# Performance work log

Hardware: AMD Instinct MI355X
Metric: run time of the kernel (lower is better)

The kernel has to match this reference:

```python
import jax, jax.numpy as jnp
import numpy as np

N, E, CIN, A, C, NB, B = 20000, 100000, 64, 32, 256, 4, 128
FD = C * NB  # fusion_dims = channels + c_growth*(n_blocks_out-1) with c_growth==channels
HID = 1024


def setup_inputs() -> dict:
    key = jax.random.key(0)
    ks = jax.random.split(key, 24)
    s = 0.05
    inp = {
        "x": jax.random.normal(ks[0], (N, CIN), jnp.float32),
        "edges": jax.random.randint(ks[1], (2, E), 0, N, jnp.int32),
        "edge_weights": jax.random.uniform(ks[2], (E,), jnp.float32),
        "edge_attrs": jax.random.normal(ks[3], (E, A), jnp.float32),
        "bbox_idx": jax.random.randint(ks[4], (N,), 0, B, jnp.int32),
        "num_boxes": B,
        # head GraphConv params: message MLP on [x_dst, x_src-x_dst, edge_attr]
        "W_msg0": jax.random.normal(ks[5], (2 * CIN + A, C), jnp.float32) * s,
        "b_msg0": jnp.zeros((C,), jnp.float32),
        "W_sup0": jax.random.normal(ks[6], (C + CIN, C), jnp.float32) * s,
        "b_sup0": jnp.zeros((C,), jnp.float32),
        # ResBlock params (n_blocks-1 blocks)
        "W_msg": jax.random.normal(ks[7], (NB - 1, 2 * C + A, C), jnp.float32) * s,
        "b_msg": jnp.zeros((NB - 1, C), jnp.float32),
        "W_sup": jax.random.normal(ks[8], (NB - 1, 2 * C, C), jnp.float32) * s,
        "b_sup": jnp.zeros((NB - 1, C), jnp.float32),
        # fusion MLPs [fusion_dims -> 1024]
        "W_fuse": jax.random.normal(ks[9], (FD, HID), jnp.float32) * s,
        "b_fuse": jnp.zeros((HID,), jnp.float32),
        "W_fuse_sup": jax.random.normal(ks[10], (FD, HID), jnp.float32) * s,
        "b_fuse_sup": jnp.zeros((HID,), jnp.float32),
    }
    return inp


def reference(x, edge_weights, edge_attrs, W_msg0, b_msg0, W_sup0, b_sup0,
              W_msg, b_msg, W_sup, b_sup, W_fuse, b_fuse, W_fuse_sup, b_fuse_sup,
              edges, bbox_idx, num_boxes):
    src, dst = edges[0], edges[1]
    n = x.shape[0]

    def gconv(f_in, Wm, bm):
        # per-edge message on [f_dst, f_src - f_dst, edge_attr], weighted sum-aggregate to dst
        h = jnp.concatenate([f_in[dst], f_in[src] - f_in[dst], edge_attrs], axis=1)
        m = jax.nn.relu(h @ Wm + bm) * edge_weights[:, None]
        return jax.ops.segment_sum(m, dst, num_segments=n)

    def super_node(f, x_node, Ws, bs):
        return jax.nn.relu(jnp.concatenate([f, x_node], axis=1) @ Ws + bs)

    # head GraphConv
    f = gconv(x, W_msg0, b_msg0)
    fs = super_node(f, x, W_sup0, b_sup0)
    feats, feats_super = [f], [fs]
    # ResBlocks: residual on node features, fresh super features
    for i in range(NB - 1):
        f = gconv(feats[-1], W_msg[i], b_msg[i]) + feats[-1]
        fs = super_node(f, feats_super[-1], W_sup[i], b_sup[i])
        feats.append(f)
        feats_super.append(fs)

    # n_blocks_out == n_blocks -> take all blocks
    feats_cat = jnp.concatenate(feats, axis=1)            # [N, FD]
    fusion = jax.nn.relu(feats_cat @ W_fuse + b_fuse)     # [N, 1024]
    out_feat = jnp.concatenate([fusion, feats_cat], axis=1)

    fs_cat = jnp.concatenate(feats_super, axis=1)         # [N, FD]
    sums = jax.ops.segment_sum(fs_cat, bbox_idx, num_segments=num_boxes)
    cnts = jax.ops.segment_sum(jnp.ones((n, 1), fs_cat.dtype), bbox_idx, num_segments=num_boxes)
    fs_mean = sums / jnp.maximum(cnts, 1.0)               # scatter(reduce='mean')
    fusion_sup = jax.nn.relu(fs_mean @ W_fuse_sup + b_fuse_sup)
    out_feat_super = jnp.concatenate([fusion_sup, fs_mean], axis=1)
    return out_feat, out_feat_super
```

## Files before the change

### kernel.cpp

```cpp
#include <hip/hip_runtime.h>

#define N_NODES 20000
#define N_EDGES 100000
#define CIN     64
#define A_DIM   32
#define CCH     256
#define NBOX    128
#define FD      1024
#define HID     1024
#define OUT_STRIDE 2048

typedef __attribute__((ext_vector_type(8))) short          short8;
typedef __attribute__((ext_vector_type(8))) unsigned short ushort8;
typedef __attribute__((ext_vector_type(4))) unsigned short ushort4v;
typedef __attribute__((ext_vector_type(4))) float          floatx4;

__device__ __forceinline__ unsigned short f2bf(float f) {
    unsigned int u = __float_as_uint(f);
    u += 0x7fff + ((u >> 16) & 1);
    return (unsigned short)(u >> 16);
}
__device__ __forceinline__ float bf2f(unsigned short h) {
    return __uint_as_float(((unsigned int)h) << 16);
}

__device__ __forceinline__ void glds16(const unsigned short* g, unsigned short* l) {
    __builtin_amdgcn_global_load_lds(
        (const __attribute__((address_space(1))) unsigned int*)g,
        (__attribute__((address_space(3))) unsigned int*)l,
        16, 0, 0);
}

struct GD {
    const unsigned short* src0b;
    const unsigned short* src1b;
    const unsigned short* Wt;
    const float* bias;
    const int* ridx0;
    float* outf;
    unsigned short* outb;
    int s0, o0, C0, s1, o1, do_relu, sof, oof, sob, oob, rmode, M, K, nbc;
};

__global__ __launch_bounds__(256) void mfma_dense(GD A, GD B, int n0)
{
    __shared__ __align__(16) unsigned short SM[2][4096];

    const int tid = threadIdx.x;
    const bool fa = (int)blockIdx.x < n0;

    const unsigned short* src0b = fa ? A.src0b : B.src0b;
    const unsigned short* src1b = fa ? A.src1b : B.src1b;
    const unsigned short* Wt    = fa ? A.Wt    : B.Wt;
    const float* bias           = fa ? A.bias  : B.bias;
    const int*   ridx0          = fa ? A.ridx0 : B.ridx0;
    float* outf                 = fa ? A.outf  : B.outf;
    unsigned short* outb        = fa ? A.outb  : B.outb;
    const int s0  = fa ? A.s0  : B.s0,  o0  = fa ? A.o0  : B.o0;
    const int C0  = fa ? A.C0  : B.C0;
    const int s1  = fa ? A.s1  : B.s1,  o1  = fa ? A.o1  : B.o1;
    const int do_relu = fa ? A.do_relu : B.do_relu;
    const int sof = fa ? A.sof : B.sof, oof = fa ? A.oof : B.oof;
    const int sob = fa ? A.sob : B.sob, oob = fa ? A.oob : B.oob;
    const int rmode = fa ? A.rmode : B.rmode;
    const int M   = fa ? A.M   : B.M;
    const int K   = fa ? A.K   : B.K;
    const int nbc = fa ? A.nbc : B.nbc;

    const int nwg = fa ? n0 : (int)gridDim.x - n0;
    const int lb  = (int)blockIdx.x - (fa ? 0 : n0);
    const int q8  = nwg >> 3, r8 = nwg & 7;
    const int xcd = lb & 7, boff = lb >> 3;
    const int bid = (xcd < r8 ? xcd * (q8 + 1)
                              : r8 * (q8 + 1) + (xcd - r8) * q8) + boff;

    const int rb   = bid / nbc, cb = bid % nbc;
    const int r0   = rb * 128, c0 = cb * 128;
    const int wave = tid >> 6, lane = tid & 63;
    const int quad = lane >> 4, l16 = lane & 15;
    const int wm   = (wave & 1) * 64, wn = (wave >> 1) * 64;

    int arow[2], grow[2], brow[2], kch[2];
    #pragma unroll
    for (int i = 0; i < 2; ++i) {
        const int g  = i * 256 + tid;
        const int rr = g >> 2;
        kch[i] = (g & 3) << 3;
        int gr2 = r0 + rr;
        if (gr2 >= M) gr2 = M - 1;
        grow[i] = gr2;
        arow[i] = ridx0 ? ridx0[gr2] : gr2;
        brow[i] = c0 + rr;
    }
    unsigned short* AsW = &SM[0][wave * 512];
    unsigned short* BsW = &SM[1][wave * 512];

    floatx4 acc[4][4];
    #pragma unroll
    for (int i = 0; i < 4; ++i)
        #pragma unroll
        for (int j = 0; j < 4; ++j) acc[i][j] = (floatx4){0.f, 0.f, 0.f, 0.f};

    const unsigned short* pB0 = Wt + (long)brow[0] * K + kch[0];
    const unsigned short* pB1 = Wt + (long)brow[1] * K + kch[1];

    auto KSTEP = [&](const unsigned short* pA0, const unsigned short* pA1) {
        glds16(pA0, AsW);
        glds16(pB0, BsW);
        glds16(pA1, AsW + 2048);
        glds16(pB1, BsW + 2048);
        __syncthreads();

        short8 af[4], bfr[4];
        #pragma unroll
        for (int mt = 0; mt < 4; ++mt)
            af[mt] = *(const short8*)(&SM[0][(wm + mt * 16 + l16) * 32 + quad * 8]);
        #pragma unroll
        for (int nt = 0; nt < 4; ++nt)
            bfr[nt] = *(const short8*)(&SM[1][(wn + nt * 16 + l16) * 32 + quad * 8]);
        #pragma unroll
        for (int mt = 0; mt < 4; ++mt)
            #pragma unroll
            for (int nt = 0; nt < 4; ++nt)
                acc[mt][nt] = __builtin_amdgcn_mfma_f32_16x16x32_bf16(
                    af[mt], bfr[nt], acc[mt][nt], 0, 0, 0);
        __syncthreads();
        pB0 += 32; pB1 += 32;
    };

    int k0 = 0;
    const int Ka = (C0 < K) ? C0 : K;
    if (k0 < Ka) {
        const unsigned short* pA0 = src0b + (long)arow[0] * s0 + o0 + kch[0];
        const unsigned short* pA1 = src0b + (long)arow[1] * s0 + o0 + kch[1];
        for (; k0 < Ka; k0 += 32) {
            KSTEP(pA0, pA1);
            pA0 += 32; pA1 += 32;
        }
    }
    if (k0 < K) {
        const unsigned short* pA0 = src1b + (long)grow[0] * s1 + o1 + kch[0];
        const unsigned short* pA1 = src1b + (long)grow[1] * s1 + o1 + kch[1];
        for (; k0 < K; k0 += 32) {
            KSTEP(pA0, pA1);
            pA0 += 32; pA1 += 32;
        }
    }

    if (outf) {
        #pragma unroll
        for (int nt = 0; nt < 4; ++nt) {
            const int gc = c0 + wn + nt * 16 + l16;
            const float bv = bias ? bias[gc] : 0.f;
            #pragma unroll
            for (int mt = 0; mt < 4; ++mt) {
                #pragma unroll
                for (int reg = 0; reg < 4; ++reg) {
                    const int grr = r0 + wm + mt * 16 + quad * 4 + reg;
                    if (grr < M) {
                        float v = acc[mt][nt][reg] + bv;
                        if (do_relu) v = fmaxf(v, 0.f);
                        outf[(long)grr * sof + oof + gc] = v;
                    }
                }
            }
        }
    }
    if (outb) {
        unsigned short* Cs = &SM[0][0];
        #pragma unroll
        for (int p = 0; p < 2; ++p) {
            if (wm == p * 64) {
                #pragma unroll
                for (int nt = 0; nt < 4; ++nt) {
                    const int col = wn + nt * 16 + l16;
                    const float bv = bias ? bias[c0 + col] : 0.f;
                    #pragma unroll
                    for (int mt = 0; mt < 4; ++mt) {
                        #pragma unroll
                        for (int reg = 0; reg < 4; ++reg) {
                            float v = acc[mt][nt][reg] + bv;
                            if (do_relu) v = fmaxf(v, 0.f);
                            Cs[(mt * 16 + quad * 4 + reg) * 128 + col] = f2bf(v);
                        }
                    }
                }
            }
            __syncthreads();
            const int rl  = tid >> 2;
            const int cc0 = (tid & 3) << 3;
            const int grr2 = r0 + p * 64 + rl;
            if (grr2 < M) {
                const long rowbase = (rmode == 2)
                    ? ((long)(c0 >> 8) * ((long)N_EDGES * 256)
                       + (long)grr2 * 256 + (c0 & 255))
                    : ((long)grr2 * sob + oob + c0);
                #pragma unroll
                for (int j = 0; j < 4; ++j)
                    *(ushort8*)(outb + rowbase + cc0 + j * 32) =
                        *(const ushort8*)(&Cs[rl * 128 + cc0 + j * 32]);
            }
            __syncthreads();
        }
    }
}

__global__ __launch_bounds__(256) void agg_kernel(
    const unsigned short* __restrict__ pq,
    const int* __restrict__ rowptr,
    const int* __restrict__ ssrc,
    const float* __restrict__ sew,
    const unsigned short* __restrict__ Rb,
    const float* __restrict__ resid,
    const float* __restrict__ bias,
    float* __restrict__ out, int fofs, int rofs,
    unsigned short* __restrict__ nfbf, int nofs)
{
    const int wid  = (blockIdx.x * blockDim.x + threadIdx.x) >> 6;
    const int lane = threadIdx.x & 63;
    if (wid >= N_NODES) return;
    const int c = lane * 4;

    const ushort4v p4 = *(const ushort4v*)(pq + (long)wid * 512 + c);
    const float4 bb = *(const float4*)(bias + c);
    float pb[4] = {bf2f(p4[0]) + bb.x, bf2f(p4[1]) + bb.y,
                   bf2f(p4[2]) + bb.z, bf2f(p4[3]) + bb.w};
    float acc[4] = {0.f, 0.f, 0.f, 0.f};

    int s = rowptr[wid];
    const int sEnd = rowptr[wid + 1];

    ushort4v qA, rA, qB, rB;
    float wA = 0.f, wB = 0.f;
    if (s < sEnd) {
        const int n_ = ssrc[s];
        wA = sew[s];
        qA = *(const ushort4v*)(pq + (long)n_ * 512 + 256 + c);
        rA = *(const ushort4v*)(Rb + (long)s * 256 + c);
    }
    if (s + 1 < sEnd) {
        const int n_ = ssrc[s + 1];
        wB = sew[s + 1];
        qB = *(const ushort4v*)(pq + (long)n_ * 512 + 256 + c);
        rB = *(const ushort4v*)(Rb + (long)(s + 1) * 256 + c);
    }
    while (s + 1 < sEnd) {
        #pragma unroll
        for (int j = 0; j < 4; ++j)
            acc[j] += fmaxf(pb[j] + bf2f(qA[j]) + bf2f(rA[j]), 0.f) * wA;
        if (s + 2 < sEnd) {
            const int n_ = ssrc[s + 2];
            wA = sew[s + 2];
            qA = *(const ushort4v*)(pq + (long)n_ * 512 + 256 + c);
            rA = *(const ushort4v*)(Rb + (long)(s + 2) * 256 + c);
        }
        #pragma unroll
        for (int j = 0; j < 4; ++j)
            acc[j] += fmaxf(pb[j] + bf2f(qB[j]) + bf2f(rB[j]), 0.f) * wB;
        if (s + 3 < sEnd) {
            const int n_ = ssrc[s + 3];
            wB = sew[s + 3];
            qB = *(const ushort4v*)(pq + (long)n_ * 512 + 256 + c);
            rB = *(const ushort4v*)(Rb + (long)(s + 3) * 256 + c);
        }
        s += 2;
    }
    if (s < sEnd) {
        #pragma unroll
        for (int j = 0; j < 4; ++j)
            acc[j] += fmaxf(pb[j] + bf2f(qA[j]) + bf2f(rA[j]), 0.f) * wA;
    }
    if (rofs >= 0) {
        const float4 f4 = *(const float4*)(resid + (long)wid * OUT_STRIDE + rofs + c);
        acc[0] += f4.x; acc[1] += f4.y; acc[2] += f4.z; acc[3] += f4.w;
    }
    float4 o; o.x = acc[0]; o.y = acc[1]; o.z = acc[2]; o.w = acc[3];
    *(float4*)(out + (long)wid * OUT_STRIDE + fofs + c) = o;
    ushort4v hb = (ushort4v){f2bf(acc[0]), f2bf(acc[1]), f2bf(acc[2]), f2bf(acc[3])};
    *(ushort4v*)(nfbf + (long)wid * FD + nofs + c) = hb;
}

__device__ __forceinline__ void tr_block(const float* inp, unsigned short* outp,
                                         int K, int N, int bidx, int tid,
                                         float (*tile)[33])
{
    const int nbx = N >> 5;
    const int n0 = (bidx % nbx) << 5;
    const int k0 = (bidx / nbx) << 5;
    const int tx = tid & 31, ty = tid >> 5;
    #pragma unroll
    for (int r = 0; r < 4; ++r)
        tile[ty + r * 8][tx] = inp[(long)(k0 + ty + r * 8) * N + n0 + tx];
    __syncthreads();
    #pragma unroll
    for (int r = 0; r < 4; ++r)
        outp[(long)(n0 + ty + r * 8) * K + k0 + tx] = f2bf(tile[tx][ty + r * 8]);
}

#define PB_ZERO  79
#define PB_CVTX  1250
#define PB_CVTE  3125
#define PB_WPQ0  128
#define PB_WPQ3  384
#define PB_WTR   128
#define PB_TS0   80
#define PB_TS3   384
#define PB_TF    1024
#define PREP_BLOCKS (PB_ZERO+PB_CVTX+PB_CVTE+PB_WPQ0+PB_WPQ3+PB_WTR+PB_TS0+PB_TS3+PB_TF+PB_TF)

__global__ __launch_bounds__(256) void prep_all(
    const float* __restrict__ x, const float* __restrict__ ea,
    const float* __restrict__ W_msg0, const float* __restrict__ W_msg,
    const float* __restrict__ W_sup0, const float* __restrict__ W_sup,
    const float* __restrict__ W_fuse, const float* __restrict__ W_fsup,
    unsigned short* __restrict__ xb, unsigned short* __restrict__ eab,
    unsigned short* __restrict__ wpq0, unsigned short* __restrict__ wpq,
    unsigned short* __restrict__ wtr,
    unsigned short* __restrict__ wt_sup0, unsigned short* __restrict__ wt_sup,
    unsigned short* __restrict__ wt_fuse, unsigned short* __restrict__ wt_fsup,
    int* __restrict__ cnt, int* __restrict__ bcnt)
{
    __shared__ float tile[32][33];
    const int tid = threadIdx.x;
    int b = blockIdx.x;

    if (b < PB_ZERO) {
        int i = b * 256 + tid;
        if (i < N_NODES + 1) cnt[i] = 0;
        else if (i - (N_NODES + 1) < 129) bcnt[i - (N_NODES + 1)] = 0;
        return;
    }
    b -= PB_ZERO;
    if (b < PB_CVTX) {
        int i = b * 256 + tid;
        float4 v = ((const float4*)x)[i];
        ((ushort4v*)xb)[i] = (ushort4v){f2bf(v.x), f2bf(v.y), f2bf(v.z), f2bf(v.w)};
        return;
    }
    b -= PB_CVTX;
    if (b < PB_CVTE) {
        int i = b * 256 + tid;
        float4 v = ((const float4*)ea)[i];
        ((ushort4v*)eab)[i] = (ushort4v){f2bf(v.x), f2bf(v.y), f2bf(v.z), f2bf(v.w)};
        return;
    }
    b -= PB_CVTE;
    if (b < PB_WPQ0) {
        int i = b * 256 + tid;
        int nn = i >> 6, k = i & 63;
        float v = (nn < 256) ? (W_msg0[k * 256 + nn] - W_msg0[(64 + k) * 256 + nn])
                             : (W_msg0[(64 + k) * 256 + (nn - 256)]);
        wpq0[(long)nn * 64 + k] = f2bf(v);
        return;
    }
    b -= PB_WPQ0;
    if (b < PB_WPQ3) {
        const int slab = b / 128, bb = b % 128;
        const float* Wi = W_msg + (long)slab * 544 * 256;
        unsigned short* Wo = wpq + (long)slab * 512 * 256;
        const int n0 = (bb & 15) << 5;
        const int k0 = (bb >> 4) << 5;
        const int tx = tid & 31, ty = tid >> 5;
        #pragma unroll
        for (int r = 0; r < 4; ++r) {
            const int k = k0 + ty + r * 8;
            float v;
            if (n0 < 256)
                v = Wi[(long)k * 256 + n0 + tx] - Wi[(long)(256 + k) * 256 + n0 + tx];
            else
                v = Wi[(long)(256 + k) * 256 + (n0 - 256) + tx];
            tile[ty + r * 8][tx] = v;
        }
        __syncthreads();
        #pragma unroll
        for (int r = 0; r < 4; ++r)
            Wo[(long)(n0 + ty + r * 8) * 256 + k0 + tx] = f2bf(tile[tx][ty + r * 8]);
        return;
    }
    b -= PB_WPQ3;
    if (b < PB_WTR) {
        const int j = b >> 5;
        const float* Wi = (j == 0) ? (W_msg0 + 2 * CIN * 256)
                                   : (W_msg + (long)(j - 1) * 544 * 256 + 2 * CCH * 256);
        unsigned short* Wo = wtr + (long)j * 256 * 32;
        int i = (b & 31) * 256 + tid;
        int k = i >> 8, n = i & 255;
        Wo[(long)n * 32 + k] = f2bf(Wi[i]);
        return;
    }
    b -= PB_WTR;
    if (b < PB_TS0) { tr_block(W_sup0, wt_sup0, 320, 256, b, tid, tile); return; }
    b -= PB_TS0;
    if (b < PB_TS3) {
        const int slab = b / 128;
        tr_block(W_sup + (long)slab * 512 * 256, wt_sup + (long)slab * 256 * 512,
                 512, 256, b % 128, tid, tile);
        return;
    }
    b -= PB_TS3;
    if (b < PB_TF) { tr_block(W_fuse, wt_fuse, 1024, 1024, b, tid, tile); return; }
    b -= PB_TF;
    tr_block(W_fsup, wt_fsup, 1024, 1024, b, tid, tile);
}

__global__ void hist2(const int* __restrict__ dst, const int* __restrict__ bbox,
                      int* __restrict__ cnt, int* __restrict__ bcnt) {
    int i = blockIdx.x * blockDim.x + threadIdx.x;
    if (i < N_EDGES) atomicAdd(&cnt[dst[i]], 1);
    else if (i - N_EDGES < N_NODES) atomicAdd(&bcnt[bbox[i - N_EDGES]], 1);
}
__global__ __launch_bounds__(1024) void scan2(
    const int* __restrict__ cnt,  int* __restrict__ rowptr, int* __restrict__ ofs,
    const int* __restrict__ bcnt, int* __restrict__ bptr,   int* __restrict__ bofs)
{
    __shared__ int part[1024];
    const int tid = threadIdx.x;
    const int n = blockIdx.x == 0 ? N_NODES : NBOX;
    const int* c   = blockIdx.x == 0 ? cnt    : bcnt;
    int* rp        = blockIdx.x == 0 ? rowptr : bptr;
    int* op        = blockIdx.x == 0 ? ofs    : bofs;
    const int chunk = (n + 1023) >> 10;
    int s = 0;
    for (int j = 0; j < chunk; ++j) {
        int i = tid * chunk + j;
        if (i < n) s += c[i];
    }
    part[tid] = s; __syncthreads();
    for (int d = 1; d < 1024; d <<= 1) {
        int v = (tid >= d) ? part[tid - d] : 0;
        __syncthreads();
        part[tid] += v;
        __syncthreads();
    }
    int run = (tid > 0) ? part[tid - 1] : 0;
    for (int j = 0; j < chunk; ++j) {
        int i = tid * chunk + j;
        if (i < n) { rp[i] = run; op[i] = run; run += c[i]; }
    }
    if (tid == 1023) rp[n] = part[1023];
}
__global__ void scatter2(const int* __restrict__ src, const int* __restrict__ dst,
                         const float* __restrict__ ew, int* __restrict__ ofs,
                         int* __restrict__ ssrc, float* __restrict__ sew,
                         int* __restrict__ seid,
                         const int* __restrict__ bbox, int* __restrict__ bofs,
                         int* __restrict__ snode) {
    int i = blockIdx.x * blockDim.x + threadIdx.x;
    if (i < N_EDGES) {
        int pos = atomicAdd(&ofs[dst[i]], 1);
        ssrc[pos] = src[i];
        sew[pos]  = ew[i];
        seid[pos] = i;
    } else if (i - N_EDGES < N_NODES) {
        int j = i - N_EDGES;
        int pos = atomicAdd(&bofs[bbox[j]], 1);
        snode[pos] = j;
    }
}

__global__ __launch_bounds__(256) void box_mean_csr(
    const unsigned short* __restrict__ fsbf, const int* __restrict__ bptr,
    const int* __restrict__ snode, float* __restrict__ out_super,
    unsigned short* __restrict__ fsmeanb)
{
    const int b = blockIdx.x >> 2;
    const int c = ((blockIdx.x & 3) << 8) + threadIdx.x;
    const int s0 = bptr[b], s1 = bptr[b + 1];
    float sum = 0.f;
    int s = s0;
    unsigned short hn = 0;
    if (s < s1) hn = fsbf[(long)snode[s] * FD + c];
    while (s < s1) {
        const unsigned short h = hn;
        if (s + 1 < s1) hn = fsbf[(long)snode[s + 1] * FD + c];
        sum += bf2f(h);
        ++s;
    }
    const float mean = sum / fmaxf((float)(s1 - s0), 1.f);
    out_super[(long)b * OUT_STRIDE + HID + c] = mean;
    fsmeanb[(long)b * FD + c] = f2bf(mean);
}

extern "C" void kernel_launch(void* const* d_in, const int* in_sizes, int n_in,
                              void* d_out, int out_size, void* d_ws, size_t ws_size,
                              hipStream_t stream) {
    const float* x      = (const float*)d_in[0];
    const int*   edges  = (const int*)d_in[1];
    const float* ew     = (const float*)d_in[2];
    const float* ea     = (const float*)d_in[3];
    const int*   bbox   = (const int*)d_in[4];
    const float* W_msg0 = (const float*)d_in[6];
    const float* b_msg0 = (const float*)d_in[7];
    const float* W_sup0 = (const float*)d_in[8];
    const float* b_sup0 = (const float*)d_in[9];
    const float* W_msg  = (const float*)d_in[10];
    const float* b_msg  = (const float*)d_in[11];
    const float* W_sup  = (const float*)d_in[12];
    const float* b_sup  = (const float*)d_in[13];
    const float* W_fuse = (const float*)d_in[14];
    const float* b_fuse = (const float*)d_in[15];
    const float* W_fsup = (const float*)d_in[16];
    const float* b_fsup = (const float*)d_in[17];

    float* out       = (float*)d_out;
    float* out_super = out + (long)N_NODES * OUT_STRIDE;

    char* w = (char*)d_ws;
    auto alloc = [&](size_t bytes) { char* p = w; w += (bytes + 63) & ~63ULL; return p; };
    unsigned short* fsbf    = (unsigned short*)alloc((size_t)N_NODES * FD * 2);
    unsigned short* nfbf    = (unsigned short*)alloc((size_t)N_NODES * FD * 2);
    unsigned short* pq      = (unsigned short*)alloc((size_t)N_NODES * 512 * 2);
    unsigned short* xb      = (unsigned short*)alloc((size_t)N_NODES * CIN * 2);
    unsigned short* eab     = (unsigned short*)alloc((size_t)N_EDGES * A_DIM * 2);
    unsigned short* Rb4     = (unsigned short*)alloc((size_t)N_EDGES * 1024 * 2);
    unsigned short* wpq0    = (unsigned short*)alloc((size_t)512 * CIN * 2);
    unsigned short* wpq     = (unsigned short*)alloc((size_t)3 * 512 * CCH * 2);
    unsigned short* wtr     = (unsigned short*)alloc((size_t)4 * 256 * 32 * 2);
    unsigned short* wt_sup0 = (unsigned short*)alloc((size_t)256 * 320 * 2);
    unsigned short* wt_sup  = (unsigned short*)alloc((size_t)3 * 256 * 512 * 2);
    unsigned short* wt_fuse = (unsigned short*)alloc((size_t)1024 * 1024 * 2);
    unsigned short* wt_fsup = (unsigned short*)alloc((size_t)1024 * 1024 * 2);
    unsigned short* fsmeanb = (unsigned short*)alloc((size_t)NBOX * FD * 2);
    float* sew        = (float*)alloc((size_t)N_EDGES * 4);
    int* cnt          = (int*)alloc((size_t)(N_NODES + 1) * 4);
    int* rowptr       = (int*)alloc((size_t)(N_NODES + 1) * 4);
    int* ofs          = (int*)alloc((size_t)(N_NODES + 1) * 4);
    int* ssrc         = (int*)alloc((size_t)N_EDGES * 4);
    int* seid         = (int*)alloc((size_t)N_EDGES * 4);
    int* bcnt         = (int*)alloc(129 * 4);
    int* bptr         = (int*)alloc(129 * 4);
    int* bofs         = (int*)alloc(129 * 4);
    int* snode        = (int*)alloc((size_t)N_NODES * 4);

    const int* srcp = edges;
    const int* dstp = edges + N_EDGES;

    prep_all<<<PREP_BLOCKS, 256, 0, stream>>>(
        x, ea, W_msg0, W_msg, W_sup0, W_sup, W_fuse, W_fsup,
        xb, eab, wpq0, wpq, wtr, wt_sup0, wt_sup, wt_fuse, wt_fsup,
        cnt, bcnt);

    hist2<<<(N_EDGES + N_NODES + 255) / 256, 256, 0, stream>>>(dstp, bbox, cnt, bcnt);
    scan2<<<2, 1024, 0, stream>>>(cnt, rowptr, ofs, bcnt, bptr, bofs);
    scatter2<<<(N_EDGES + N_NODES + 255) / 256, 256, 0, stream>>>(
        srcp, dstp, ew, ofs, ssrc, sew, seid, bbox, bofs, snode);

    const int GRB = (N_NODES + 127) / 128;
    const int GEB = (N_EDGES + 127) / 128;
    const long RLS = (long)N_EDGES * 256;

    auto mk = [](const unsigned short* src0b, int s0, int o0, int C0,
                 const int* ridx0,
                 const unsigned short* src1b, int s1, int o1,
                 const unsigned short* Wt, const float* bias, int relu,
                 float* outf, int sof, int oof,
                 unsigned short* outb, int sob, int oob, int rmode,
                 int M, int K, int nbc) {
        GD g;
        g.src0b = src0b; g.s0 = s0; g.o0 = o0; g.C0 = C0;
        g.ridx0 = ridx0;
        g.src1b = src1b; g.s1 = s1; g.o1 = o1;
        g.Wt = Wt; g.bias = bias; g.do_relu = relu;
        g.outf = outf; g.sof = sof; g.oof = oof;
        g.outb = outb; g.sob = sob; g.oob = oob; g.rmode = rmode;
        g.M = M; g.K = K; g.nbc = nbc;
        return g;
    };

    GD gR   = mk(eab, A_DIM, 0, A_DIM, seid, nullptr, 0, 0, wtr, nullptr, 0,
                 nullptr, 0, 0, Rb4, 0, 0, 2, N_EDGES, A_DIM, 8);
    GD gPQh = mk(xb, CIN, 0, CIN, nullptr, nullptr, 0, 0, wpq0, nullptr, 0,
                 nullptr, 0, 0, pq, 512, 0, 0, N_NODES, CIN, 4);
    GD gS0  = mk(nfbf, FD, 0, CCH, nullptr, xb, CIN, 0, wt_sup0, b_sup0, 1,
                 nullptr, 0, 0, fsbf, FD, 0, 0, N_NODES, CCH + CIN, 2);
    GD gPQ[3], gS[3];
    for (int i = 0; i < 3; ++i) {
        gPQ[i] = mk(nfbf, FD, CCH * i, CCH, nullptr, nullptr, 0, 0,
                    wpq + (long)i * 512 * CCH, nullptr, 0,
                    nullptr, 0, 0, pq, 512, 0, 0, N_NODES, CCH, 4);
        gS[i]  = mk(nfbf, FD, CCH * (i + 1), CCH, nullptr, fsbf, FD, CCH * i,
                    wt_sup + (long)i * 256 * 512, b_sup + i * CCH, 1,
                    nullptr, 0, 0, fsbf, FD, CCH * (i + 1), 0, N_NODES, 2 * CCH, 2);
    }
    GD gFU  = mk(nfbf, FD, 0, FD, nullptr, nullptr, 0, 0, wt_fuse, b_fuse, 1,
                 out, OUT_STRIDE, 0, nullptr, 0, 0, 0, N_NODES, FD, 8);
    GD gFS  = mk(fsmeanb, FD, 0, FD, nullptr, nullptr, 0, 0, wt_fsup, b_fsup, 1,
                 out_super, OUT_STRIDE, 0, nullptr, 0, 0, 0, NBOX, FD, 8);

    const int AGRID = (N_NODES + 3) / 4;

    mfma_dense<<<GEB * 8 + GRB * 4, 256, 0, stream>>>(gR, gPQh, GEB * 8);

    agg_kernel<<<AGRID, 256, 0, stream>>>(pq, rowptr, ssrc, sew,
        Rb4, out, b_msg0, out, HID, -1, nfbf, 0);

    mfma_dense<<<GRB * 6, 256, 0, stream>>>(gS0, gPQ[0], GRB * 2);
    for (int i = 0; i < 3; ++i) {
        agg_kernel<<<AGRID, 256, 0, stream>>>(pq, rowptr, ssrc, sew,
            Rb4 + (long)(i + 1) * RLS, out, b_msg + i * CCH,
            out, HID + CCH * (i + 1), HID + CCH * i, nfbf, CCH * (i + 1));
        if (i < 2)
            mfma_dense<<<GRB * 6, 256, 0, stream>>>(gS[i], gPQ[i + 1], GRB * 2);
    }

    mfma_dense<<<GRB * 10, 256, 0, stream>>>(gS[2], gFU, GRB * 2);

    box_mean_csr<<<NBOX * 4, 256, 0, stream>>>(fsbf, bptr, snode, out_super, fsmeanb);
    mfma_dense<<<8, 256, 0, stream>>>(gFS, gFS, 8);
}
```

Baseline: 782.0 us.

## Double-buffer LDS tiles in MFMA GEMM with prefetch two steps ahead

Reworks the dense MFMA GEMM main loop to use two LDS buffers for A and B and issue the global-to-LDS loads for tile t+2 while tile t is computed. Explicit vmcnt waits and raw s_barrier calls replace the two __syncthreads per K-step, so memory latency can overlap with MFMA work. LDS use doubles to 32KB per block, which may reduce occupancy, and the hand-managed waitcnt logic relies on exact counts of outstanding loads.

```diff
diff --git a/kernel.cpp b/kernel.cpp
--- a/kernel.cpp
+++ b/kernel.cpp
@@ -44,7 +44,7 @@
 
 __global__ __launch_bounds__(256) void mfma_dense(GD A, GD B, int n0)
 {
-    __shared__ __align__(16) unsigned short SM[2][4096];
+    __shared__ __align__(16) unsigned short SM[16384];
 
     const int tid = threadIdx.x;
     const bool fa = (int)blockIdx.x < n0;
@@ -92,8 +92,6 @@
         arow[i] = ridx0 ? ridx0[gr2] : gr2;
         brow[i] = c0 + rr;
     }
-    unsigned short* AsW = &SM[0][wave * 512];
-    unsigned short* BsW = &SM[1][wave * 512];
 
     floatx4 acc[4][4];
     #pragma unroll
@@ -101,50 +99,58 @@
         #pragma unroll
         for (int j = 0; j < 4; ++j) acc[i][j] = (floatx4){0.f, 0.f, 0.f, 0.f};
 
-    const unsigned short* pB0 = Wt + (long)brow[0] * K + kch[0];
-    const unsigned short* pB1 = Wt + (long)brow[1] * K + kch[1];
-
-    auto KSTEP = [&](const unsigned short* pA0, const unsigned short* pA1) {
-        glds16(pA0, AsW);
-        glds16(pB0, BsW);
-        glds16(pA1, AsW + 2048);
-        glds16(pB1, BsW + 2048);
-        __syncthreads();
-
+    auto stage_tile = [&](int ts) {
+        const int kk = ts << 5;
+        const unsigned short *a0, *a1;
+        if (kk < C0) {
+            a0 = src0b + (long)arow[0] * s0 + o0 + kk + kch[0];
+            a1 = src0b + (long)arow[1] * s0 + o0 + kk + kch[1];
+        } else {
+            a0 = src1b + (long)grow[0] * s1 + o1 + (kk - C0) + kch[0];
+            a1 = src1b + (long)grow[1] * s1 + o1 + (kk - C0) + kch[1];
+        }
+        const unsigned short* b0 = Wt + (long)brow[0] * K + kk + kch[0];
+        const unsigned short* b1 = Wt + (long)brow[1] * K + kk + kch[1];
+        const int buf = ts & 1;
+        glds16(a0, &SM[buf * 4096 + wave * 512]);
+        glds16(b0, &SM[8192 + buf * 4096 + wave * 512]);
+        glds16(a1, &SM[buf * 4096 + wave * 512 + 2048]);
+        glds16(b1, &SM[8192 + buf * 4096 + wave * 512 + 2048]);
+    };
+
+    const int NT = K >> 5;
+    stage_tile(0);
+    if (NT > 1) stage_tile(1);
+
+    for (int t = 0; t < NT; ++t) {
+        if (t + 1 < NT)
+            asm volatile("s_waitcnt vmcnt(4)" ::: "memory");
+        else
+            asm volatile("s_waitcnt vmcnt(0)" ::: "memory");
+        __builtin_amdgcn_s_barrier();
+        __builtin_amdgcn_sched_barrier(0);
+
+        const int buf = t & 1;
         short8 af[4], bfr[4];
         #pragma unroll
         for (int mt = 0; mt < 4; ++mt)
-            af[mt] = *(const short8*)(&SM[0][(wm + mt * 16 + l16) * 32 + quad * 8]);
+            af[mt] = *(const short8*)(
+                &SM[buf * 4096 + (wm + mt * 16 + l16) * 32 + quad * 8]);
         #pragma unroll
         for (int nt = 0; nt < 4; ++nt)
-            bfr[nt] = *(const short8*)(&SM[1][(wn + nt * 16 + l16) * 32 + quad * 8]);
+            bfr[nt] = *(const short8*)(
+                &SM[8192 + buf * 4096 + (wn + nt * 16 + l16) * 32 + quad * 8]);
         #pragma unroll
         for (int mt = 0; mt < 4; ++mt)
             #pragma unroll
             for (int nt = 0; nt < 4; ++nt)
                 acc[mt][nt] = __builtin_amdgcn_mfma_f32_16x16x32_bf16(
                     af[mt], bfr[nt], acc[mt][nt], 0, 0, 0);
-        __syncthreads();
-        pB0 += 32; pB1 += 32;
-    };
-
-    int k0 = 0;
-    const int Ka = (C0 < K) ? C0 : K;
-    if (k0 < Ka) {
-        const unsigned short* pA0 = src0b + (long)arow[0] * s0 + o0 + kch[0];
-        const unsigned short* pA1 = src0b + (long)arow[1] * s0 + o0 + kch[1];
-        for (; k0 < Ka; k0 += 32) {
-            KSTEP(pA0, pA1);
-            pA0 += 32; pA1 += 32;
-        }
-    }
-    if (k0 < K) {
-        const unsigned short* pA0 = src1b + (long)grow[0] * s1 + o1 + kch[0];
-        const unsigned short* pA1 = src1b + (long)grow[1] * s1 + o1 + kch[1];
-        for (; k0 < K; k0 += 32) {
-            KSTEP(pA0, pA1);
-            pA0 += 32; pA1 += 32;
-        }
+
+        asm volatile("s_waitcnt lgkmcnt(0)" ::: "memory");
+        __builtin_amdgcn_sched_barrier(0);
+        __builtin_amdgcn_s_barrier();
+        if (t + 2 < NT) stage_tile(t + 2);
     }
 
     if (outf) {
@@ -167,7 +173,8 @@
         }
     }
     if (outb) {
-        unsigned short* Cs = &SM[0][0];
+        unsigned short* Cs = &SM[0];
+        __syncthreads();
         #pragma unroll
         for (int p = 0; p < 2; ++p) {
             if (wm == p * 64) {
```

Result: faster. 754.4 us (-3.5%).
